# Kernel tuning notes

Hardware: AMD Instinct MI355X
Metric: run time of the kernel (lower is better)

Reference implementation:

```python
import jax, jax.numpy as jnp
import numpy as np

DIST = 200.0
BBOX_SP = 24
N_COARSE = 64
N_BOXES = 10
SAMPLES_ALL = N_COARSE + 2 * N_BOXES  # 84
FR_POS = 10
FR_DIR = 4
NSEM = 50
WID = 256
MERGES = [(39, 41), (27, 26), (28, 26), (29, 26), (30, 26), (31, 26), (9, 8), (35, 13)]


def posenc(x, L):
    f = 2.0 ** jnp.arange(L, dtype=x.dtype)
    xb = x[..., None, :] * f[:, None]                      # [..., L, 3]
    enc = jnp.concatenate([jnp.sin(xb), jnp.cos(xb)], -1)  # [..., L, 6]
    return jnp.concatenate([x, enc.reshape(x.shape[:-1] + (-1,))], -1)


def sample_pdf(bins, weights, n):
    # deterministic inverse-CDF sampling (det=True), bins [B,N,M], weights [B,N,M-1]
    pdf = weights / jnp.sum(weights, -1, keepdims=True)
    cdf = jnp.cumsum(pdf, -1)
    cdf = jnp.concatenate([jnp.zeros_like(cdf[..., :1]), cdf], -1)   # [B,N,M]
    B, N, M = cdf.shape
    u = jnp.linspace(0.0, 1.0, n, dtype=bins.dtype)
    cdf_f = cdf.reshape(B * N, M)
    bins_f = bins.reshape(B * N, M)
    u_f = jnp.broadcast_to(u, (B * N, n))
    inds = jax.vmap(lambda c, uu: jnp.searchsorted(c, uu, side='right'))(cdf_f, u_f)
    below = jnp.clip(inds - 1, 0, M - 1)
    above = jnp.clip(inds, 0, M - 1)
    cdf_b = jnp.take_along_axis(cdf_f, below, 1)
    cdf_a = jnp.take_along_axis(cdf_f, above, 1)
    bin_b = jnp.take_along_axis(bins_f, below, 1)
    bin_a = jnp.take_along_axis(bins_f, above, 1)
    denom = jnp.where(cdf_a - cdf_b < 1e-5, 1.0, cdf_a - cdf_b)
    t = (u_f - cdf_b) / denom
    return (bin_b + t * (bin_a - bin_b)).reshape(B, N, n)


def setup_inputs() -> dict:
    key = jax.random.key(0)
    ks = jax.random.split(key, 16)
    B, N = 1, 2048
    rays_o = jax.random.normal(ks[0], (B, N, 3)) * 2.0
    rays_d = jax.random.normal(ks[1], (B, N, 3))
    rays = jnp.concatenate([rays_o, rays_d], -1)
    near = jax.random.uniform(ks[2], (B, N, N_BOXES), minval=5.0, maxval=150.0)
    far = near + jax.random.uniform(ks[3], (B, N, N_BOXES), minval=5.0, maxval=60.0)
    inst = jax.random.randint(ks[4], (B, N, N_BOXES), 0, 20).astype(jnp.float32)
    label = jax.random.randint(ks[5], (B, N, N_BOXES), 1, NSEM).astype(jnp.float32)
    intersection = jnp.stack([near, far, inst, label], -1)  # [B,N,10,4]
    bg_noise = jax.random.uniform(ks[6], (B, N, SAMPLES_ALL))

    def lin(k, fi, fo):
        return jax.random.normal(k, (fi, fo)) / np.sqrt(fi)

    d_x = 3 + 6 * FR_POS  # 63
    d_d = 3 + 6 * FR_DIR  # 27
    params = dict(
        w_in=lin(ks[7], d_x, WID), b_in=jnp.zeros((WID,)),
        w_h=jax.random.normal(ks[8], (6, WID, WID)) / np.sqrt(WID), b_h=jnp.zeros((6, WID)),
        w_skip=lin(ks[9], WID + d_x, WID), b_skip=jnp.zeros((WID,)),
        w_sigma=lin(ks[10], WID, 1), b_sigma=jnp.zeros((1,)),
        w_feat=lin(ks[11], WID, WID), b_feat=jnp.zeros((WID,)),
        w_rgb1=lin(ks[12], WID + d_d, 128), b_rgb1=jnp.zeros((128,)),
        w_rgb2=lin(ks[13], 128, 3), b_rgb2=jnp.zeros((3,)),
        w_sem=lin(ks[14], WID, NSEM), b_sem=jnp.zeros((NSEM,)),
    )
    out = {'rays': rays, 'intersection': intersection, 'bg_noise': bg_noise}
    out.update(params)
    return out


def reference(rays, intersection, bg_noise, w_in, b_in, w_h, b_h, w_skip, b_skip,
              w_sigma, b_sigma, w_feat, b_feat, w_rgb1, b_rgb1, w_rgb2, b_rgb2,
              w_sem, b_sem):
    B, N, _ = rays.shape
    rays_o, rays_d = rays[..., :3], rays[..., 3:6]
    scale = jnp.linalg.norm(rays_d, axis=-1)  # [B,N]

    # --- ray sampling inside boxes + uniform-PDF resampling ---
    near, far = intersection[..., 0], intersection[..., 1]  # [B,N,10]
    t = jnp.linspace(0.0, 1.0, BBOX_SP)
    z_box = near[..., None] + (far - near)[..., None] * t       # [B,N,10,24]
    z_bound = jnp.concatenate([z_box[..., 0] - 1e-5, z_box[..., -1] + 1e-5], axis=2)  # [B,N,20]
    zf = jnp.sort(z_box.reshape(B, N, -1), axis=2)              # [B,N,240]
    z = sample_pdf(zf, jnp.ones_like(zf[..., 1:]), N_COARSE)    # [B,N,64]
    z = jnp.concatenate([z, z_bound], axis=2)                   # [B,N,84]
    z = jnp.where(z < 0.0, DIST + 20.0 * bg_noise, z)
    z = jnp.sort(z, axis=2)

    # --- NeRF MLP on sample points ---
    xyz = (rays_o[:, :, None] + rays_d[:, :, None] * z[..., None] / scale[..., None, None]) / DIST
    dirs = rays_d / scale[..., None]
    x_enc = posenc(xyz, FR_POS)                                 # [B,N,S,63]
    h = jax.nn.relu(x_enc @ w_in + b_in)
    for i in range(3):
        h = jax.nn.relu(h @ w_h[i] + b_h[i])
    h = jax.nn.relu(jnp.concatenate([h, x_enc], -1) @ w_skip + b_skip)
    for i in range(3, 6):
        h = jax.nn.relu(h @ w_h[i] + b_h[i])
    sigma = (h @ w_sigma + b_sigma)[..., 0]                     # [B,N,S]
    sem = h @ w_sem + b_sem                                     # [B,N,S,50]
    feat = h @ w_feat + b_feat
    d_enc = posenc(dirs, FR_DIR)                                # [B,N,27]
    d_enc = jnp.broadcast_to(d_enc[:, :, None, :], feat.shape[:-1] + (d_enc.shape[-1],))
    hr = jax.nn.relu(jnp.concatenate([feat, d_enc], -1) @ w_rgb1 + b_rgb1)
    rgb = hr @ w_rgb2 + b_rgb2                                  # [B,N,S,3]

    # --- semantic one-hot scatter + boundary masks (no-grad region) ---
    zs = jax.lax.stop_gradient(z)
    nearb = intersection[:, :, None, :, 0]                      # [B,N,1,10]
    farb = intersection[:, :, None, :, 1]
    inside = (zs[..., None] > nearb) & (zs[..., None] < farb)   # [B,N,S,10]
    d1 = zs[..., None] - farb
    d2 = nearb - zs[..., None]
    mask_bound = jnp.any(((d1 > 0) & (d1 < 1e-3)) | ((d2 > 0) & (d2 < 1e-3)), axis=-1)
    labels = intersection[..., 3].astype(jnp.int32)             # [B,N,10]
    oh_box = jax.nn.one_hot(labels, NSEM)                       # [B,N,10,50]
    one_hot = jnp.max(inside[..., None].astype(jnp.float32) * oh_box[:, :, None, :, :], axis=3)
    s0 = one_hot.sum(-1)
    mask_bbox = (zs < DIST) & (s0 == 0.0)
    mask_bg = (zs > DIST) & (s0 == 0.0)
    one_hot = one_hot.at[..., 0].set(jnp.where(mask_bbox, 1.0, one_hot[..., 0]))
    one_hot = one_hot.at[..., 23].set(jnp.where(mask_bg, 1.0, one_hot[..., 23]))
    for src, dst in MERGES:  # training-mode class merging (box/car/park/gate)
        one_hot = one_hot.at[..., dst].set(jnp.maximum(one_hot[..., dst], one_hot[..., src]))
        one_hot = one_hot.at[..., src].set(0.0)
    one_hot = jax.lax.stop_gradient(one_hot)

    # zero density outside boxes and at box boundaries
    sigma = jnp.where(mask_bbox | mask_bound, 0.0, sigma)

    # --- volumetric compositing (raw2outputs_semantic_joint) ---
    z_true = z / scale[..., None]
    dists = jnp.concatenate([z_true[..., 1:] - z_true[..., :-1],
                             jnp.full_like(z_true[..., :1], 1e10)], -1) * scale[..., None]
    alpha = 1.0 - jnp.exp(-jax.nn.relu(sigma) * dists)
    trans = jnp.cumprod(jnp.concatenate([jnp.ones_like(alpha[..., :1]),
                                         1.0 - alpha + 1e-10], -1)[..., :-1], -1)
    w = alpha * trans                                           # [B,N,S]
    rgb_map = jnp.einsum('bns,bnsc->bnc', w, jax.nn.sigmoid(rgb))
    depth = jnp.sum(w * z_true, -1)
    acc = jnp.sum(w, -1)
    sem_map = jnp.einsum('bns,bnsc->bnc', w, sem)
    return jnp.concatenate([rgb_map, depth[..., None], acc[..., None], sem_map], -1)  # [B,N,55]
```

## Files before the change

### kernel.cpp

```cpp
#include <hip/hip_runtime.h>

typedef _Float16 half8 __attribute__((ext_vector_type(8)));
typedef float f32x4 __attribute__((ext_vector_type(4)));

#define NRAYS 2048
#define SAMP 84
#define NPTS (NRAYS*SAMP)
#define SEMSTR 52

#define WT0_OFF   0
#define WTH_OFF   16384
#define WTS_OFF   409600
#define WTHD_OFF  491520
#define WTR1_OFF  573440
#define WTR2_OFF  610304
#define WT_TOTAL  612352
#define NBIAS     2512

#define OFF_WT    ((size_t)0)
#define OFF_BIAS  ((size_t)1224704)
#define OFF_Z     (OFF_BIAS + (size_t)NBIAS*4)
#define OFF_SCALE (OFF_Z + (size_t)NPTS*4)
#define OFF_SIGMA (OFF_SCALE + (size_t)NRAYS*4)
#define OFF_RGB   (OFF_SIGMA + (size_t)NPTS*4)
#define OFF_SEM   (OFF_RGB + (size_t)NPTS*12)

__global__ __launch_bounds__(256) void prep_kernel(
    const float* __restrict__ w_in,  const float* __restrict__ w_h,
    const float* __restrict__ w_skip,const float* __restrict__ w_sigma,
    const float* __restrict__ w_feat,const float* __restrict__ w_rgb1,
    const float* __restrict__ w_rgb2,const float* __restrict__ w_sem,
    const float* __restrict__ b_in,  const float* __restrict__ b_h,
    const float* __restrict__ b_skip,const float* __restrict__ b_sigma,
    const float* __restrict__ b_feat,const float* __restrict__ b_rgb1,
    const float* __restrict__ b_rgb2,const float* __restrict__ b_sem,
    _Float16* __restrict__ wt, float* __restrict__ bias)
{
  int idx = blockIdx.x*256 + threadIdx.x;
  if (idx < WT_TOTAL) {
    float v; int n, k, l, h, q;
    if (idx < WTH_OFF) {
      int r = idx; int F = r >> 10; int rem = r & 1023; int kt = rem >> 9; q = rem & 511;
      l = q >> 3; h = q & 7;
      n = F*16 + (l&15); k = kt*32 + (l>>4)*8 + h;
      v = (k < 63) ? w_in[k*256 + n] : 0.f;
    } else if (idx < WTS_OFF) {
      int r = idx - WTH_OFF; int i = r >> 16; int r2 = r & 65535;
      int F = r2 >> 12; int kt = (r2 >> 9) & 7; q = r2 & 511;
      l = q >> 3; h = q & 7;
      n = F*16 + (l&15); k = kt*32 + (l>>4)*8 + h;
      v = w_h[(i<<16) + (k<<8) + n];
    } else if (idx < WTHD_OFF) {
      int r = idx - WTS_OFF; int F = r / 5120; int rem = r % 5120; int kt = rem >> 9; q = rem & 511;
      l = q >> 3; h = q & 7;
      n = F*16 + (l&15); k = kt*32 + (l>>4)*8 + h;
      v = (k < 319) ? w_skip[k*256 + n] : 0.f;
    } else if (idx < WTR1_OFF) {
      int r = idx - WTHD_OFF; int F = r >> 12; int kt = (r >> 9) & 7; q = r & 511;
      l = q >> 3; h = q & 7;
      n = F*16 + (l&15); k = kt*32 + (l>>4)*8 + h;
      v = (n < 256) ? w_feat[(k<<8) + n]
        : (n < 306) ? w_sem[k*50 + (n-256)]
        : (n == 306)? w_sigma[k] : 0.f;
    } else if (idx < WTR2_OFF) {
      int r = idx - WTR1_OFF; int F = r / 4608; int rem = r % 4608; int kt = rem >> 9; q = rem & 511;
      l = q >> 3; h = q & 7;
      n = F*16 + (l&15); k = kt*32 + (l>>4)*8 + h;
      v = (k < 283) ? w_rgb1[k*128 + n] : 0.f;
    } else {
      int r = idx - WTR2_OFF; int kt = r >> 9; q = r & 511;
      l = q >> 3; h = q & 7;
      n = (l&15); k = kt*32 + (l>>4)*8 + h;
      v = (n < 3) ? w_rgb2[k*3 + n] : 0.f;
    }
    wt[idx] = (_Float16)v;
  } else if (idx < WT_TOTAL + NBIAS) {
    int j = idx - WT_TOTAL; float v;
    if (j < 2048) {
      int i = j >> 8, c = j & 255;
      v = (i==0) ? b_in[c] : (i<4) ? b_h[(i-1)*256+c]
        : (i==4) ? b_skip[c] : b_h[(i-2)*256+c];
    } else if (j < 2368) {
      int c = j - 2048;
      v = (c<256) ? b_feat[c] : (c<306) ? b_sem[c-256]
        : (c==306) ? b_sigma[0] : 0.f;
    } else if (j < 2496) v = b_rgb1[j-2368];
    else { int c = j-2496; v = (c<3) ? b_rgb2[c] : 0.f; }
    bias[j] = v;
  }
}

__global__ __launch_bounds__(256) void sample_kernel(
    const float* __restrict__ rays, const float* __restrict__ inter,
    const float* __restrict__ noise, float* __restrict__ zbuf,
    float* __restrict__ scaleb)
{
  __shared__ float sv[240], ss[240], z2[84];
  const int ray = blockIdx.x, t = threadIdx.x;
  const float* bx = inter + (size_t)ray*40;
  if (t < 240) {
    int b = t/24, j = t%24;
    float nr = bx[b*4], fr = bx[b*4+1];
    float tj = (j==23) ? 1.f : (float)j * (1.f/23.f);
    sv[t] = nr + (fr-nr)*tj;
  }
  __syncthreads();
  if (t < 240) {
    float v = sv[t]; int r = 0;
    for (int i = 0; i < 240; ++i) { float vi = sv[i]; r += (vi < v) || (vi == v && i < t); }
    ss[r] = v;
  }
  __syncthreads();
  if (t < 64) {
    float z;
    if (t == 63) z = ss[239];
    else { int num = t*239; int k = num/63; float f = (float)(num - k*63)*(1.f/63.f);
           z = ss[k] + f*(ss[k+1]-ss[k]); }
    z2[t] = z;
  } else if (t < 84) {
    int b = t - 64;
    z2[t] = (b < 10) ? (bx[b*4] - 1e-5f) : (bx[(b-10)*4+1] + 1e-5f);
  }
  __syncthreads();
  if (t < 84) { float z = z2[t]; if (z < 0.f) z = 200.f + 20.f*noise[(size_t)ray*84 + t]; z2[t] = z; }
  __syncthreads();
  if (t < 84) {
    float v = z2[t]; int r = 0;
    for (int i = 0; i < 84; ++i) { float vi = z2[i]; r += (vi < v) || (vi == v && i < t); }
    zbuf[(size_t)ray*84 + r] = v;
  }
  if (t == 0) {
    float dx = rays[ray*6+3], dy = rays[ray*6+4], dz = rays[ray*6+5];
    scaleb[ray] = sqrtf(dx*dx + dy*dy + dz*dz);
  }
}

#define LDS_A 0u
#define LDS_B 32768u
#define LDS_X 65536u
#define LDS_TOTAL 73728

__device__ __forceinline__ uint32_t laddr(uint32_t base, int m, int k) {
  return base + (uint32_t)(m*512) + (uint32_t)((((k>>3)^(m&7))<<4) + ((k&7)<<1));
}
__device__ __forceinline__ uint32_t laddrX(int m, int k) {
  return LDS_X + (uint32_t)(m*128) + (uint32_t)(((((k>>3)&7)^(m&7))<<4) + ((k&7)<<1));
}
struct __attribute__((aligned(8))) H4 { _Float16 h[4]; };

__device__ __forceinline__ float xenc_val(int j, float x0, float x1, float x2) {
  if (j >= 63) return 0.f;
  if (j < 3) return j==0?x0:(j==1?x1:x2);
  int q = j-3, lf = q/6, r = q%6, ci = r%3;
  float xc = (ci==0)?x0:((ci==1)?x1:x2);
  float arg = xc * (float)(1<<lf);
  return (r<3) ? sinf(arg) : cosf(arg);
}
__device__ __forceinline__ float denc_val(int c, float u0, float u1, float u2) {
  if (c >= 27) return 0.f;
  if (c < 3) return c==0?u0:(c==1?u1:u2);
  int q = c-3, lf = q/6, r = q%6, ci = r%3;
  float uc = (ci==0)?u0:((ci==1)?u1:u2);
  float arg = uc * (float)(1<<lf);
  return (r<3) ? sinf(arg) : cosf(arg);
}

template<int KT, int NF, int MF, int MODE, bool RELU, int XSTART>
__device__ __forceinline__ void gemm(uint8_t* smem, uint32_t inb, uint32_t outb,
    const _Float16* __restrict__ WT, int fbase, const float* __restrict__ biasptr,
    int p0, float* __restrict__ sigmaws, _Float16* __restrict__ semws)
{
  const int t = threadIdx.x;
  const int l = t & 63, w = t >> 6;
  const int lr = l & 15, lg = l >> 4;
  const int wn = w >> 1, wm = w & 1;
  const int m0 = wm*(MF*16);
  constexpr int DW = (KT < 3) ? KT : 3;
  f32x4 acc[NF][MF];
#pragma unroll
  for (int i = 0; i < NF; ++i)
#pragma unroll
    for (int j = 0; j < MF; ++j) acc[i][j] = (f32x4){0.f,0.f,0.f,0.f};
  const _Float16* wb = WT + (size_t)((fbase + wn*NF)*KT)*512 + (size_t)l*8;
  half8 av[DW][NF];
  half8 bv[2][MF];
  auto baddr = [&](int row, int kt)->uint32_t {
    const int kk = kt*32 + lg*8;
    if (XSTART == 0) return laddrX(row, kk);
    if (XSTART < 100000 && kt*32 >= XSTART) return laddrX(row, kk - XSTART);
    return laddr(inb, row, kk);
  };
#pragma unroll
  for (int d = 0; d < DW; ++d)
#pragma unroll
    for (int nf = 0; nf < NF; ++nf)
      av[d][nf] = *(const half8*)(wb + (size_t)(nf*KT + d)*512);
#pragma unroll
  for (int mf = 0; mf < MF; ++mf)
    bv[0][mf] = *(const half8*)(smem + baddr(m0 + mf*16 + lr, 0));
#pragma unroll
  for (int kt = 0; kt < KT; ++kt) {
    if (kt + 1 < KT) {
#pragma unroll
      for (int mf = 0; mf < MF; ++mf)
        bv[(kt+1)&1][mf] = *(const half8*)(smem + baddr(m0 + mf*16 + lr, kt+1));
    }
    __builtin_amdgcn_sched_barrier(0);
#pragma unroll
    for (int nf = 0; nf < NF; ++nf)
#pragma unroll
      for (int mf = 0; mf < MF; ++mf)
        acc[nf][mf] = __builtin_amdgcn_mfma_f32_16x16x32_f16(av[kt%DW][nf], bv[kt&1][mf], acc[nf][mf], 0, 0, 0);
    __builtin_amdgcn_sched_barrier(0);
    if (kt + DW < KT) {
#pragma unroll
      for (int nf = 0; nf < NF; ++nf)
        av[kt%DW][nf] = *(const half8*)(wb + (size_t)(nf*KT + kt + DW)*512);
    }
  }
#pragma unroll
  for (int nf = 0; nf < NF; ++nf) {
    if (MODE == 0) {
      const int n0 = wn*(NF*16) + nf*16;
      const int nb = n0 + lg*4;
      const f32x4 bvv = *(const f32x4*)(biasptr + nb);
#pragma unroll
      for (int mf = 0; mf < MF; ++mf) {
        const int m = m0 + mf*16 + lr;
        f32x4 v = acc[nf][mf] + bvv;
        H4 hh;
#pragma unroll
        for (int r = 0; r < 4; ++r) { float x = v[r]; if (RELU) x = fmaxf(x, 0.f); hh.h[r] = (_Float16)x; }
        *(H4*)(smem + laddr(outb, m, nb)) = hh;
      }
    } else {
      const int cb = wn*(NF*16) + nf*16 + lg*4;
      const f32x4 bvv = *(const f32x4*)(biasptr + cb);
#pragma unroll
      for (int mf = 0; mf < MF; ++mf) {
        const int m = m0 + mf*16 + lr;
        const int pp = p0 + m;
        f32x4 v = acc[nf][mf] + bvv;
        if (cb <= 44) {
          H4 hh;
#pragma unroll
          for (int r = 0; r < 4; ++r) hh.h[r] = (_Float16)v[r];
          *(H4*)(semws + (size_t)pp*SEMSTR + cb) = hh;
        } else if (cb == 48) {
          semws[(size_t)pp*SEMSTR + 48] = (_Float16)v[0];
          semws[(size_t)pp*SEMSTR + 49] = (_Float16)v[1];
          sigmaws[pp] = v[2];
        }
      }
    }
  }
}

__device__ __forceinline__ void gemm_rgb2(uint8_t* smem, uint32_t inb,
    const _Float16* __restrict__ WT, const float* __restrict__ bias,
    int p0, float* __restrict__ rgbws)
{
  const int t = threadIdx.x;
  const int l = t & 63, w = t >> 6;
  const int lr = l & 15, lg = l >> 4;
  const int m0 = w*16;
  f32x4 acc = (f32x4){0.f,0.f,0.f,0.f};
#pragma unroll
  for (int kt = 0; kt < 4; ++kt) {
    const int kk = kt*32 + lg*8;
    half8 a = *(const half8*)(WT + (size_t)kt*512 + (size_t)l*8);
    half8 b = *(const half8*)(smem + laddr(inb, m0 + lr, kk));
    acc = __builtin_amdgcn_mfma_f32_16x16x32_f16(a, b, acc, 0, 0, 0);
  }
  const int pp = p0 + m0 + lr;
#pragma unroll
  for (int r = 0; r < 4; ++r) {
    const int n = lg*4 + r;
    if (n < 3) rgbws[(size_t)pp*3 + n] = (float)acc[r] + bias[n];
  }
}

__global__ __launch_bounds__(256,2) void mlp_kernel(
    const float* __restrict__ rays, const float* __restrict__ zbuf,
    const float* __restrict__ scaleb, const _Float16* __restrict__ wt,
    const float* __restrict__ bias, float* __restrict__ sigmaws,
    float* __restrict__ rgbws, _Float16* __restrict__ semws)
{
  extern __shared__ uint8_t smem[];
  const int p0 = blockIdx.x*64;
  const int t = threadIdx.x;
  const int m = t & 63, g = t >> 6;
  const int p = p0 + m;
  const int ray = p / SAMP;
  const float sc = scaleb[ray];
  const float z  = zbuf[p];
  const float ox = rays[ray*6+0], oy = rays[ray*6+1], oz = rays[ray*6+2];
  const float dx = rays[ray*6+3], dy = rays[ray*6+4], dz = rays[ray*6+5];
  const float x0 = (ox + dx*z/sc)/200.f;
  const float x1 = (oy + dy*z/sc)/200.f;
  const float x2 = (oz + dz*z/sc)/200.f;
  const float u0 = dx/sc, u1 = dy/sc, u2 = dz/sc;
  {
    union { _Float16 hv[8]; half8 v; } u8;
#pragma unroll
    for (int half = 0; half < 2; ++half) {
      const int j0 = g*16 + half*8;
#pragma unroll
      for (int jj = 0; jj < 8; ++jj) u8.hv[jj] = (_Float16)xenc_val(j0+jj, x0, x1, x2);
      *(half8*)(smem + laddrX(m, j0)) = u8.v;
    }
  }
  __syncthreads();
  gemm<2 ,8,2,0,true ,0     >(smem, LDS_X, LDS_A, wt+WT0_OFF,         0,  bias+0,    p0, sigmaws, semws); __syncthreads();
  gemm<8 ,8,2,0,true ,100000>(smem, LDS_A, LDS_B, wt+WTH_OFF+0*65536, 0,  bias+256,  p0, sigmaws, semws); __syncthreads();
  gemm<8 ,8,2,0,true ,100000>(smem, LDS_B, LDS_A, wt+WTH_OFF+1*65536, 0,  bias+512,  p0, sigmaws, semws); __syncthreads();
  gemm<8 ,8,2,0,true ,100000>(smem, LDS_A, LDS_B, wt+WTH_OFF+2*65536, 0,  bias+768,  p0, sigmaws, semws); __syncthreads();
  gemm<10,8,2,0,true ,256   >(smem, LDS_B, LDS_A, wt+WTS_OFF,         0,  bias+1024, p0, sigmaws, semws); __syncthreads();
  if (g < 4) {
    union { _Float16 hv[8]; half8 v; } u8;
    const int c0 = g*8;
#pragma unroll
    for (int cc = 0; cc < 8; ++cc) u8.hv[cc] = (_Float16)denc_val(c0+cc, u0, u1, u2);
    *(half8*)(smem + laddrX(m, c0)) = u8.v;
  }
  gemm<8 ,8,2,0,true ,100000>(smem, LDS_A, LDS_B, wt+WTH_OFF+3*65536, 0,  bias+1280, p0, sigmaws, semws); __syncthreads();
  gemm<8 ,8,2,0,true ,100000>(smem, LDS_B, LDS_A, wt+WTH_OFF+4*65536, 0,  bias+1536, p0, sigmaws, semws); __syncthreads();
  gemm<8 ,8,2,0,true ,100000>(smem, LDS_A, LDS_B, wt+WTH_OFF+5*65536, 0,  bias+1792, p0, sigmaws, semws); __syncthreads();
  gemm<8 ,8,2,0,false,100000>(smem, LDS_B, LDS_A, wt+WTHD_OFF,        0,  bias+2048, p0, sigmaws, semws);
  gemm<8 ,2,2,1,false,100000>(smem, LDS_B, LDS_A, wt+WTHD_OFF,        16, bias+2304, p0, sigmaws, semws); __syncthreads();
  gemm<9 ,4,2,0,true ,256   >(smem, LDS_A, LDS_B, wt+WTR1_OFF,        0,  bias+2368, p0, sigmaws, semws); __syncthreads();
  gemm_rgb2(smem, LDS_B, wt+WTR2_OFF, bias+2496, p0, rgbws);
}

__global__ __launch_bounds__(128) void comp_kernel(
    const float* __restrict__ inter, const float* __restrict__ zbuf,
    const float* __restrict__ scaleb, const float* __restrict__ sigmaws,
    const float* __restrict__ rgbws, const _Float16* __restrict__ semws,
    float* __restrict__ out)
{
  __shared__ float zt[84], alpha[84], wgt[84];
  const int ray = blockIdx.x, t = threadIdx.x;
  const float sc = scaleb[ray];
  const float* bx = inter + (size_t)ray*40;
  if (t < 84) zt[t] = zbuf[(size_t)ray*84 + t] / sc;
  __syncthreads();
  if (t < 84) {
    const float z = zbuf[(size_t)ray*84 + t];
    bool inside = false, bound = false;
    for (int b = 0; b < 10; ++b) {
      const float nr = bx[b*4], fr = bx[b*4+1];
      inside = inside || (z > nr && z < fr);
      const float d1 = z - fr, d2 = nr - z;
      bound = bound || (d1 > 0.f && d1 < 1e-3f) || (d2 > 0.f && d2 < 1e-3f);
    }
    float sg = sigmaws[(size_t)ray*84 + t];
    const bool bbox = (z < 200.f) && !inside;
    if (bbox || bound) sg = 0.f;
    sg = fmaxf(sg, 0.f);
    const float dist = (t < 83) ? (zt[t+1] - zt[t])*sc : 1e10f*sc;
    alpha[t] = 1.f - expf(-sg*dist);
  }
  __syncthreads();
  if (t == 0) {
    float T = 1.f;
    for (int s = 0; s < 84; ++s) { wgt[s] = alpha[s]*T; T *= (1.f - alpha[s] + 1e-10f); }
  }
  __syncthreads();
  if (t < 55) {
    float a = 0.f;
    const size_t base = (size_t)ray*84;
    if (t < 50) {
      for (int s = 0; s < 84; ++s) a += wgt[s]*(float)semws[(base+s)*SEMSTR + t];
      out[(size_t)ray*55 + 5 + t] = a;
    } else if (t < 53) {
      const int c = t - 50;
      for (int s = 0; s < 84; ++s) { const float r = rgbws[(base+s)*3 + c]; a += wgt[s]/(1.f + expf(-r)); }
      out[(size_t)ray*55 + c] = a;
    } else if (t == 53) {
      for (int s = 0; s < 84; ++s) a += wgt[s]*zt[s];
      out[(size_t)ray*55 + 3] = a;
    } else {
      for (int s = 0; s < 84; ++s) a += wgt[s];
      out[(size_t)ray*55 + 4] = a;
    }
  }
}

extern "C" void kernel_launch(void* const* d_in, const int* in_sizes, int n_in,
                              void* d_out, int out_size, void* d_ws, size_t ws_size,
                              hipStream_t stream) {
  const float* rays   = (const float*)d_in[0];
  const float* inter  = (const float*)d_in[1];
  const float* noise  = (const float*)d_in[2];
  const float* w_in   = (const float*)d_in[3];
  const float* b_in   = (const float*)d_in[4];
  const float* w_h    = (const float*)d_in[5];
  const float* b_h    = (const float*)d_in[6];
  const float* w_skip = (const float*)d_in[7];
  const float* b_skip = (const float*)d_in[8];
  const float* w_sig  = (const float*)d_in[9];
  const float* b_sig  = (const float*)d_in[10];
  const float* w_feat = (const float*)d_in[11];
  const float* b_feat = (const float*)d_in[12];
  const float* w_rgb1 = (const float*)d_in[13];
  const float* b_rgb1 = (const float*)d_in[14];
  const float* w_rgb2 = (const float*)d_in[15];
  const float* b_rgb2 = (const float*)d_in[16];
  const float* w_sem  = (const float*)d_in[17];
  const float* b_sem  = (const float*)d_in[18];

  uint8_t* ws = (uint8_t*)d_ws;
  _Float16* wt    = (_Float16*)(ws + OFF_WT);
  float* bias     = (float*)(ws + OFF_BIAS);
  float* zbuf     = (float*)(ws + OFF_Z);
  float* scaleb   = (float*)(ws + OFF_SCALE);
  float* sigmaws  = (float*)(ws + OFF_SIGMA);
  float* rgbws    = (float*)(ws + OFF_RGB);
  _Float16* semws = (_Float16*)(ws + OFF_SEM);

  prep_kernel<<<dim3((WT_TOTAL + NBIAS + 255)/256), dim3(256), 0, stream>>>(
      w_in, w_h, w_skip, w_sig, w_feat, w_rgb1, w_rgb2, w_sem,
      b_in, b_h, b_skip, b_sig, b_feat, b_rgb1, b_rgb2, b_sem, wt, bias);
  sample_kernel<<<dim3(NRAYS), dim3(256), 0, stream>>>(rays, inter, noise, zbuf, scaleb);
  mlp_kernel<<<dim3(NPTS/64), dim3(256), LDS_TOTAL, stream>>>(
      rays, zbuf, scaleb, wt, bias, sigmaws, rgbws, semws);
  comp_kernel<<<dim3(NRAYS), dim3(128), 0, stream>>>(
      inter, zbuf, scaleb, sigmaws, rgbws, semws, (float*)d_out);
}
```

Baseline: 322.0 us.

## Retile MLP GEMMs so each wave covers all 64 rows, merge head GEMMs

Changes the warp tiling in the fused MLP kernel. Each of four waves now covers all 64 point rows (MF=4) and a quarter of the output features, instead of the previous 2x2 split over rows and features. Each weight fragment loaded from global memory is therefore reused across twice as many rows, halving redundant weight traffic. The feature head and the sigma/semantic head are merged into one GEMM with mixed-mode output, which drops a separate pass. Weight prefetch is also moved ahead of the MFMA block with a configurable lead distance. The cost is more accumulator registers per wave and more LDS activation reads per wave.

```diff
diff --git a/kernel.cpp b/kernel.cpp
--- a/kernel.cpp
+++ b/kernel.cpp
@@ -165,17 +165,18 @@
   return (r<3) ? sinf(arg) : cosf(arg);
 }
 
-template<int KT, int NF, int MF, int MODE, bool RELU, int XSTART>
+template<int KT, int NF, int MODE, bool RELU, int XSTART>
 __device__ __forceinline__ void gemm(uint8_t* smem, uint32_t inb, uint32_t outb,
     const _Float16* __restrict__ WT, int fbase, const float* __restrict__ biasptr,
     int p0, float* __restrict__ sigmaws, _Float16* __restrict__ semws)
 {
+  constexpr int MF = 4;
   const int t = threadIdx.x;
   const int l = t & 63, w = t >> 6;
   const int lr = l & 15, lg = l >> 4;
-  const int wn = w >> 1, wm = w & 1;
-  const int m0 = wm*(MF*16);
-  constexpr int DW = (KT < 3) ? KT : 3;
+  const int wn = w & 3;
+  constexpr int DW   = (KT <= 3) ? KT : ((NF > 4) ? 3 : 4);
+  constexpr int LEAD = (KT <= 3) ? KT : DW - 1;
   f32x4 acc[NF][MF];
 #pragma unroll
   for (int i = 0; i < NF; ++i)
@@ -191,19 +192,24 @@
     return laddr(inb, row, kk);
   };
 #pragma unroll
-  for (int d = 0; d < DW; ++d)
+  for (int d = 0; d < LEAD && d < KT; ++d)
 #pragma unroll
     for (int nf = 0; nf < NF; ++nf)
       av[d][nf] = *(const half8*)(wb + (size_t)(nf*KT + d)*512);
 #pragma unroll
   for (int mf = 0; mf < MF; ++mf)
-    bv[0][mf] = *(const half8*)(smem + baddr(m0 + mf*16 + lr, 0));
+    bv[0][mf] = *(const half8*)(smem + baddr(mf*16 + lr, 0));
 #pragma unroll
   for (int kt = 0; kt < KT; ++kt) {
     if (kt + 1 < KT) {
 #pragma unroll
       for (int mf = 0; mf < MF; ++mf)
-        bv[(kt+1)&1][mf] = *(const half8*)(smem + baddr(m0 + mf*16 + lr, kt+1));
+        bv[(kt+1)&1][mf] = *(const half8*)(smem + baddr(mf*16 + lr, kt+1));
+    }
+    if (kt + LEAD < KT) {
+#pragma unroll
+      for (int nf = 0; nf < NF; ++nf)
+        av[(kt+LEAD)%DW][nf] = *(const half8*)(wb + (size_t)(nf*KT + kt + LEAD)*512);
     }
     __builtin_amdgcn_sched_barrier(0);
 #pragma unroll
@@ -212,21 +218,16 @@
       for (int mf = 0; mf < MF; ++mf)
         acc[nf][mf] = __builtin_amdgcn_mfma_f32_16x16x32_f16(av[kt%DW][nf], bv[kt&1][mf], acc[nf][mf], 0, 0, 0);
     __builtin_amdgcn_sched_barrier(0);
-    if (kt + DW < KT) {
-#pragma unroll
-      for (int nf = 0; nf < NF; ++nf)
-        av[kt%DW][nf] = *(const half8*)(wb + (size_t)(nf*KT + kt + DW)*512);
-    }
   }
 #pragma unroll
   for (int nf = 0; nf < NF; ++nf) {
-    if (MODE == 0) {
-      const int n0 = wn*(NF*16) + nf*16;
-      const int nb = n0 + lg*4;
-      const f32x4 bvv = *(const f32x4*)(biasptr + nb);
+    const int n0 = (wn*NF + nf)*16;
+    const int nb = n0 + lg*4;
+    const f32x4 bvv = *(const f32x4*)(biasptr + nb);
+    if (MODE == 0 || n0 < 256) {
 #pragma unroll
       for (int mf = 0; mf < MF; ++mf) {
-        const int m = m0 + mf*16 + lr;
+        const int m = mf*16 + lr;
         f32x4 v = acc[nf][mf] + bvv;
         H4 hh;
 #pragma unroll
@@ -234,11 +235,10 @@
         *(H4*)(smem + laddr(outb, m, nb)) = hh;
       }
     } else {
-      const int cb = wn*(NF*16) + nf*16 + lg*4;
-      const f32x4 bvv = *(const f32x4*)(biasptr + cb);
+      const int cb = nb - 256;
 #pragma unroll
       for (int mf = 0; mf < MF; ++mf) {
-        const int m = m0 + mf*16 + lr;
+        const int m = mf*16 + lr;
         const int pp = p0 + m;
         f32x4 v = acc[nf][mf] + bvv;
         if (cb <= 44) {
@@ -303,32 +303,31 @@
   {
     union { _Float16 hv[8]; half8 v; } u8;
 #pragma unroll
-    for (int half = 0; half < 2; ++half) {
-      const int j0 = g*16 + half*8;
+    for (int hf = 0; hf < 2; ++hf) {
+      const int j0 = g*16 + hf*8;
 #pragma unroll
       for (int jj = 0; jj < 8; ++jj) u8.hv[jj] = (_Float16)xenc_val(j0+jj, x0, x1, x2);
       *(half8*)(smem + laddrX(m, j0)) = u8.v;
     }
   }
   __syncthreads();
-  gemm<2 ,8,2,0,true ,0     >(smem, LDS_X, LDS_A, wt+WT0_OFF,         0,  bias+0,    p0, sigmaws, semws); __syncthreads();
-  gemm<8 ,8,2,0,true ,100000>(smem, LDS_A, LDS_B, wt+WTH_OFF+0*65536, 0,  bias+256,  p0, sigmaws, semws); __syncthreads();
-  gemm<8 ,8,2,0,true ,100000>(smem, LDS_B, LDS_A, wt+WTH_OFF+1*65536, 0,  bias+512,  p0, sigmaws, semws); __syncthreads();
-  gemm<8 ,8,2,0,true ,100000>(smem, LDS_A, LDS_B, wt+WTH_OFF+2*65536, 0,  bias+768,  p0, sigmaws, semws); __syncthreads();
-  gemm<10,8,2,0,true ,256   >(smem, LDS_B, LDS_A, wt+WTS_OFF,         0,  bias+1024, p0, sigmaws, semws); __syncthreads();
-  if (g < 4) {
+  gemm<2 ,4,0,true ,0     >(smem, LDS_X, LDS_A, wt+WT0_OFF,         0, bias+0,    p0, sigmaws, semws); __syncthreads();
+  gemm<8 ,4,0,true ,100000>(smem, LDS_A, LDS_B, wt+WTH_OFF+0*65536, 0, bias+256,  p0, sigmaws, semws); __syncthreads();
+  gemm<8 ,4,0,true ,100000>(smem, LDS_B, LDS_A, wt+WTH_OFF+1*65536, 0, bias+512,  p0, sigmaws, semws); __syncthreads();
+  gemm<8 ,4,0,true ,100000>(smem, LDS_A, LDS_B, wt+WTH_OFF+2*65536, 0, bias+768,  p0, sigmaws, semws); __syncthreads();
+  gemm<10,4,0,true ,256   >(smem, LDS_B, LDS_A, wt+WTS_OFF,         0, bias+1024, p0, sigmaws, semws); __syncthreads();
+  {
     union { _Float16 hv[8]; half8 v; } u8;
     const int c0 = g*8;
 #pragma unroll
     for (int cc = 0; cc < 8; ++cc) u8.hv[cc] = (_Float16)denc_val(c0+cc, u0, u1, u2);
     *(half8*)(smem + laddrX(m, c0)) = u8.v;
   }
-  gemm<8 ,8,2,0,true ,100000>(smem, LDS_A, LDS_B, wt+WTH_OFF+3*65536, 0,  bias+1280, p0, sigmaws, semws); __syncthreads();
-  gemm<8 ,8,2,0,true ,100000>(smem, LDS_B, LDS_A, wt+WTH_OFF+4*65536, 0,  bias+1536, p0, sigmaws, semws); __syncthreads();
-  gemm<8 ,8,2,0,true ,100000>(smem, LDS_A, LDS_B, wt+WTH_OFF+5*65536, 0,  bias+1792, p0, sigmaws, semws); __syncthreads();
-  gemm<8 ,8,2,0,false,100000>(smem, LDS_B, LDS_A, wt+WTHD_OFF,        0,  bias+2048, p0, sigmaws, semws);
-  gemm<8 ,2,2,1,false,100000>(smem, LDS_B, LDS_A, wt+WTHD_OFF,        16, bias+2304, p0, sigmaws, semws); __syncthreads();
-  gemm<9 ,4,2,0,true ,256   >(smem, LDS_A, LDS_B, wt+WTR1_OFF,        0,  bias+2368, p0, sigmaws, semws); __syncthreads();
+  gemm<8 ,4,0,true ,100000>(smem, LDS_A, LDS_B, wt+WTH_OFF+3*65536, 0, bias+1280, p0, sigmaws, semws); __syncthreads();
+  gemm<8 ,4,0,true ,100000>(smem, LDS_B, LDS_A, wt+WTH_OFF+4*65536, 0, bias+1536, p0, sigmaws, semws); __syncthreads();
+  gemm<8 ,4,0,true ,100000>(smem, LDS_A, LDS_B, wt+WTH_OFF+5*65536, 0, bias+1792, p0, sigmaws, semws); __syncthreads();
+  gemm<8 ,5,1,false,100000>(smem, LDS_B, LDS_A, wt+WTHD_OFF,        0, bias+2048, p0, sigmaws, semws); __syncthreads();
+  gemm<9 ,2,0,true ,256   >(smem, LDS_A, LDS_B, wt+WTR1_OFF,        0, bias+2368, p0, sigmaws, semws); __syncthreads();
   gemm_rgb2(smem, LDS_B, wt+WTR2_OFF, bias+2496, p0, rgbws);
 }
 
```

Result: faster. 272.5 us (-15.4%).
